# Performance work log

Hardware: AMD Instinct MI355X
Metric: run time of the kernel (lower is better)

## Reference

```python
import jax, jax.numpy as jnp
import numpy as np


def setup_inputs() -> dict:
    key = jax.random.key(0)
    ks = jax.random.split(key, 8)
    B, C, H, W = 4, 256, 64, 64
    C8 = C // 8
    s = 0.05
    return {
        "x": jax.random.normal(ks[0], (B, C, H, W), jnp.float32),
        "wq": jax.random.normal(ks[1], (C8, C), jnp.float32) * s,
        "bq": jax.random.normal(ks[2], (C8,), jnp.float32) * s,
        "wk": jax.random.normal(ks[3], (C8, C), jnp.float32) * s,
        "bk": jax.random.normal(ks[4], (C8,), jnp.float32) * s,
        "wv": jax.random.normal(ks[5], (C, C), jnp.float32) * s,
        "bv": jax.random.normal(ks[6], (C,), jnp.float32) * s,
        "gamma": jax.random.uniform(ks[7], (1,), jnp.float32),
    }


def reference(x, wq, bq, wk, bk, wv, bv, gamma):
    B, C, H, W = x.shape
    N = H * W
    xf = x.reshape(B, C, N)  # flatten spatial: [B, C, N]
    # 1x1 convs are channel-wise matmuls
    q = jnp.einsum("dc,bcn->bnd", wq, xf) + bq[None, None, :]  # [B, N, C/8]
    k = jnp.einsum("dc,bcn->bdn", wk, xf) + bk[None, :, None]  # [B, C/8, N]
    v = jnp.einsum("dc,bcn->bdn", wv, xf) + bv[None, :, None]  # [B, C, N]
    energy = jnp.einsum("bnd,bdm->bnm", q, k)  # [B, N, N]
    attention = jax.nn.softmax(energy, axis=-1)
    # out = value @ attention^T  -> [B, C, N]
    out = jnp.einsum("bcm,bnm->bcn", v, attention)
    out = out.reshape(B, C, H, W)
    return gamma[0] * out + x
```

## Files before the change

### kernel.cpp

```cpp
#include <hip/hip_runtime.h>
#include <hip/hip_bf16.h>
#include <stdint.h>

#define B_ 4
#define C_ 256
#define N_ 4096
#define D_ 32
#define KT 256

typedef __bf16 bf16_t;
typedef __bf16 bf16x4_t __attribute__((ext_vector_type(4)));
typedef __bf16 bf16x8_t __attribute__((ext_vector_type(8)));
typedef float  f32x4    __attribute__((ext_vector_type(4)));

__global__ __launch_bounds__(256) void cast_kernel(
    const float* __restrict__ x,
    const float* __restrict__ wq, const float* __restrict__ wk,
    const float* __restrict__ wv,
    bf16_t* __restrict__ xbT, bf16_t* __restrict__ Wb)
{
  const int bid = blockIdx.x;
  const int t = threadIdx.x;
  if (bid >= 1024) {
    const int gr = bid - 1024;
    float v;
    if (gr < 32)      v = wq[gr * C_ + t];
    else if (gr < 64) v = wk[(gr - 32) * C_ + t];
    else              v = wv[(gr - 64) * C_ + t];
    Wb[gr * C_ + t] = (bf16_t)v;
    return;
  }
  __shared__ float xs[64][65];
  const int n0 = (bid & 63) * 64;
  const int c0 = ((bid >> 6) & 3) * 64;
  const int b  = bid >> 8;

  const int lr = t >> 4;
  const int lc = (t & 15) * 4;
#pragma unroll
  for (int i = 0; i < 4; ++i) {
    const f32x4 v = *(const f32x4*)(x + ((size_t)(b * C_ + c0 + lr + i * 16)) * N_ + n0 + lc);
    xs[lr + i * 16][lc + 0] = v[0];
    xs[lr + i * 16][lc + 1] = v[1];
    xs[lr + i * 16][lc + 2] = v[2];
    xs[lr + i * 16][lc + 3] = v[3];
  }
  __syncthreads();
  const int nr = t >> 2;
  const int cb = (t & 3) * 16;
  bf16_t tmp[16];
#pragma unroll
  for (int j = 0; j < 16; ++j) tmp[j] = (bf16_t)xs[cb + j][nr];
  bf16_t* dst = xbT + ((size_t)(b * N_ + n0 + nr)) * C_ + c0 + cb;
  *(bf16x8_t*)dst       = *(bf16x8_t*)&tmp[0];
  *(bf16x8_t*)(dst + 8) = *(bf16x8_t*)&tmp[8];
}

__global__ __launch_bounds__(256) void proj_kernel(
    const bf16_t* __restrict__ Wb, const bf16_t* __restrict__ xbT,
    const float* __restrict__ bq, const float* __restrict__ bk,
    const float* __restrict__ bv,
    bf16_t* __restrict__ Qh, bf16_t* __restrict__ Kh, bf16_t* __restrict__ Vh)
{
  const int bi = blockIdx.x;
  const int b  = bi & 3;
  const int n0 = (bi >> 2) * 64;
  const int t = threadIdx.x, w = t >> 6, lane = t & 63;
  const int l4 = lane >> 4, lm = lane & 15;

  const f32x4 z4 = {0.f, 0.f, 0.f, 0.f};
  f32x4 acc[5][4];
#pragma unroll
  for (int rt = 0; rt < 5; ++rt)
#pragma unroll
    for (int ct = 0; ct < 4; ++ct) acc[rt][ct] = z4;

#pragma unroll 1
  for (int k0 = 0; k0 < C_; k0 += 64) {
    bf16x8_t af[5][2], bfr[4][2];
#pragma unroll
    for (int rt = 0; rt < 5; ++rt)
#pragma unroll
      for (int kc = 0; kc < 2; ++kc)
        af[rt][kc] = *(const bf16x8_t*)(Wb + (size_t)(w * 80 + rt * 16 + lm) * C_ + k0 + kc * 32 + l4 * 8);
#pragma unroll
    for (int ct = 0; ct < 4; ++ct)
#pragma unroll
      for (int kc = 0; kc < 2; ++kc)
        bfr[ct][kc] = *(const bf16x8_t*)(xbT + ((size_t)(b * N_ + n0 + ct * 16 + lm)) * C_ + k0 + kc * 32 + l4 * 8);
#pragma unroll
    for (int rt = 0; rt < 5; ++rt)
#pragma unroll
      for (int ct = 0; ct < 4; ++ct)
#pragma unroll
        for (int kc = 0; kc < 2; ++kc)
          acc[rt][ct] = __builtin_amdgcn_mfma_f32_16x16x32_bf16(af[rt][kc], bfr[ct][kc], acc[rt][ct], 0, 0, 0);
  }

#pragma unroll
  for (int rt = 0; rt < 5; ++rt)
#pragma unroll
    for (int r = 0; r < 4; ++r) {
      const int gr = w * 80 + rt * 16 + 4 * l4 + r;
      const float bias = (gr < 32) ? bq[gr] : (gr < 64) ? bk[gr - 32] : bv[gr - 64];
#pragma unroll
      for (int ct = 0; ct < 4; ++ct) {
        const int n = n0 + ct * 16 + lm;
        float v = acc[rt][ct][r] + bias;
        if (gr < 32) {
          v *= 1.44269504088896f;
          Qh[((size_t)(b * N_ + n)) * D_ + gr] = (bf16_t)v;
        } else if (gr < 64) {
          Kh[((size_t)(b * N_ + n)) * D_ + (gr - 32)] = (bf16_t)v;
        } else {
          Vh[((size_t)(b * C_ + (gr - 64))) * N_ + n] = (bf16_t)v;
        }
      }
    }
}

__global__ __launch_bounds__(512, 2) void attn_kernel(
    const bf16_t* __restrict__ Qh, const bf16_t* __restrict__ Kh,
    const bf16_t* __restrict__ Vh, const float* __restrict__ x,
    const float* __restrict__ gamma, float* __restrict__ out)
{
  __shared__ __align__(16) bf16_t Pl[2][64][KT];
  __shared__ __align__(16) float  Lx[64][12];

  const int bi = blockIdx.x;
  const int xcd = bi & 7, slot = bi >> 3;
  const int b  = xcd >> 1;
  const int q0 = ((xcd & 1) * 32 + slot) * 64;

  const int t = threadIdx.x, w = t >> 6, lane = t & 63;
  const int l4 = lane >> 4, lm = lane & 15;
  const int swz = (lm & 7) << 3;

  const f32x4 z4 = {0.f, 0.f, 0.f, 0.f};

  bf16x8_t qf[4];
#pragma unroll
  for (int rt = 0; rt < 4; ++rt)
    qf[rt] = *(const bf16x8_t*)(Qh + ((size_t)(b * N_ + q0 + rt * 16 + lm)) * D_ + l4 * 8);

  const bf16_t* kbase = Kh + ((size_t)(b * N_ + w * 32 + lm)) * D_ + l4 * 8;
  const bf16_t* vbase = Vh + ((size_t)(b * C_ + w * 32 + lm)) * N_ + l4 * 8;

  f32x4 acc[2][4];
#pragma unroll
  for (int ct = 0; ct < 2; ++ct)
#pragma unroll
    for (int rt = 0; rt < 4; ++rt) acc[ct][rt] = z4;
  float l_run[4] = {0.f, 0.f, 0.f, 0.f};

  bf16x8_t kf[2], kn[2];
#pragma unroll
  for (int mt = 0; mt < 2; ++mt)
    kf[mt] = *(const bf16x8_t*)(kbase + (size_t)(mt * 16) * D_);
  bf16x8_t vf0[2][2], vf1[2][2];
#pragma unroll
  for (int ct = 0; ct < 2; ++ct)
#pragma unroll
    for (int kc = 0; kc < 2; ++kc) {
      vf0[ct][kc] = *(const bf16x8_t*)(vbase + (size_t)(ct * 16) * N_ + kc * 32);
      vf1[ct][kc] = *(const bf16x8_t*)(vbase + (size_t)(ct * 16) * N_ + 64 + kc * 32);
    }

#pragma unroll 1
  for (int it = 0; it < N_ / KT; ++it) {
    const int buf = it & 1;

    f32x4 S[4][2];
#pragma unroll
    for (int rt = 0; rt < 4; ++rt)
#pragma unroll
      for (int mt = 0; mt < 2; ++mt)
        S[rt][mt] = __builtin_amdgcn_mfma_f32_16x16x32_bf16(kf[mt], qf[rt], z4, 0, 0, 0);

    const int k0n = ((it + 1) * KT) & (N_ - 1);
#pragma unroll
    for (int mt = 0; mt < 2; ++mt)
      kn[mt] = *(const bf16x8_t*)(kbase + (size_t)(k0n + mt * 16) * D_);

#pragma unroll
    for (int rt = 0; rt < 4; ++rt) {
      const int prow = rt * 16 + lm;
#pragma unroll
      for (int mt = 0; mt < 2; ++mt) {
        const float p0 = __builtin_amdgcn_exp2f(S[rt][mt][0]);
        const float p1 = __builtin_amdgcn_exp2f(S[rt][mt][1]);
        const float p2 = __builtin_amdgcn_exp2f(S[rt][mt][2]);
        const float p3 = __builtin_amdgcn_exp2f(S[rt][mt][3]);
        l_run[rt] += (p0 + p1) + (p2 + p3);
        bf16x4_t w4 = {(bf16_t)p0, (bf16_t)p1, (bf16_t)p2, (bf16_t)p3};
        *(bf16x4_t*)&Pl[buf][prow][(w * 32 + mt * 16 + 4 * l4) ^ swz] = w4;
      }
    }

    asm volatile("s_waitcnt lgkmcnt(0)" ::: "memory");
    __builtin_amdgcn_s_barrier();

#pragma unroll
    for (int s4 = 0; s4 < 4; ++s4) {
      bf16x8_t pa[4][2];
#pragma unroll
      for (int rt = 0; rt < 4; ++rt)
#pragma unroll
        for (int kc = 0; kc < 2; ++kc)
          pa[rt][kc] = *(const bf16x8_t*)&Pl[buf][rt * 16 + lm][(s4 * 64 + kc * 32 + l4 * 8) ^ swz];
      const int knx = (it * KT + (s4 + 2) * 64) & (N_ - 1);
      if ((s4 & 1) == 0) {
#pragma unroll
        for (int ct = 0; ct < 2; ++ct)
#pragma unroll
          for (int kc = 0; kc < 2; ++kc)
#pragma unroll
            for (int rt = 0; rt < 4; ++rt)
              acc[ct][rt] = __builtin_amdgcn_mfma_f32_16x16x32_bf16(vf0[ct][kc], pa[rt][kc], acc[ct][rt], 0, 0, 0);
#pragma unroll
        for (int ct = 0; ct < 2; ++ct)
#pragma unroll
          for (int kc = 0; kc < 2; ++kc)
            vf0[ct][kc] = *(const bf16x8_t*)(vbase + (size_t)(ct * 16) * N_ + knx + kc * 32);
      } else {
#pragma unroll
        for (int ct = 0; ct < 2; ++ct)
#pragma unroll
          for (int kc = 0; kc < 2; ++kc)
#pragma unroll
            for (int rt = 0; rt < 4; ++rt)
              acc[ct][rt] = __builtin_amdgcn_mfma_f32_16x16x32_bf16(vf1[ct][kc], pa[rt][kc], acc[ct][rt], 0, 0, 0);
#pragma unroll
        for (int ct = 0; ct < 2; ++ct)
#pragma unroll
          for (int kc = 0; kc < 2; ++kc)
            vf1[ct][kc] = *(const bf16x8_t*)(vbase + (size_t)(ct * 16) * N_ + knx + kc * 32);
      }
    }

#pragma unroll
    for (int mt = 0; mt < 2; ++mt) kf[mt] = kn[mt];
  }

#pragma unroll
  for (int rt = 0; rt < 4; ++rt) {
    l_run[rt] += __shfl_xor(l_run[rt], 16);
    l_run[rt] += __shfl_xor(l_run[rt], 32);
  }
  if (l4 == 0) {
#pragma unroll
    for (int rt = 0; rt < 4; ++rt) Lx[rt * 16 + lm][w] = l_run[rt];
  }
  asm volatile("s_waitcnt lgkmcnt(0)" ::: "memory");
  __builtin_amdgcn_s_barrier();

  const float g = gamma[0];
#pragma unroll
  for (int rt = 0; rt < 4; ++rt) {
    const f32x4 s0 = *(const f32x4*)&Lx[rt * 16 + lm][0];
    const f32x4 s1 = *(const f32x4*)&Lx[rt * 16 + lm][4];
    const float lt = ((s0[0] + s0[1]) + (s0[2] + s0[3])) + ((s1[0] + s1[1]) + (s1[2] + s1[3]));
    const float inv = 1.f / lt;
    const int n = q0 + rt * 16 + lm;
#pragma unroll
    for (int ct = 0; ct < 2; ++ct) {
#pragma unroll
      for (int r = 0; r < 4; ++r) {
        const int c = w * 32 + ct * 16 + 4 * l4 + r;
        const size_t idx = ((size_t)(b * C_ + c)) * N_ + n;
        out[idx] = g * (acc[ct][rt][r] * inv) + x[idx];
      }
    }
  }
}

extern "C" void kernel_launch(void* const* d_in, const int* in_sizes, int n_in,
                              void* d_out, int out_size, void* d_ws, size_t ws_size,
                              hipStream_t stream) {
  const float* x     = (const float*)d_in[0];
  const float* wq    = (const float*)d_in[1];
  const float* bq    = (const float*)d_in[2];
  const float* wk    = (const float*)d_in[3];
  const float* bk    = (const float*)d_in[4];
  const float* wv    = (const float*)d_in[5];
  const float* bv    = (const float*)d_in[6];
  const float* gamma = (const float*)d_in[7];
  float* out = (float*)d_out;

  bf16_t* Qh  = (bf16_t*)d_ws;
  bf16_t* Kh  = Qh + (size_t)B_ * N_ * D_;
  bf16_t* Vh  = Kh + (size_t)B_ * N_ * D_;
  bf16_t* Wb  = Vh + (size_t)B_ * C_ * N_;
  bf16_t* xbT = Wb + (size_t)320 * C_;

  cast_kernel<<<1344, 256, 0, stream>>>(x, wq, wk, wv, xbT, Wb);
  proj_kernel<<<256, 256, 0, stream>>>(Wb, xbT, bq, bk, bv, Qh, Kh, Vh);
  attn_kernel<<<256, 512, 0, stream>>>(Qh, Kh, Vh, x, gamma, out);
}
```

Baseline: 94.84 us.

## Split attention key range in two and combine partial outputs

Splits the key dimension into two halves so attention launches 512 blocks instead of 256, each covering half the keys. Every block writes a bf16 normalized partial output and its row sums, and a new combine kernel merges the two halves weighted by those sums, then applies gamma and the residual. The aim is more blocks per device and higher occupancy (launch bounds raised to 4 per CU). The cost is an extra kernel launch, extra global traffic for the partials, and bf16 rounding of the intermediate output.

```diff
diff --git a/kernel.cpp b/kernel.cpp
--- a/kernel.cpp
+++ b/kernel.cpp
@@ -7,6 +7,7 @@
 #define N_ 4096
 #define D_ 32
 #define KT 256
+#define KH 2048
 
 typedef __bf16 bf16_t;
 typedef __bf16 bf16x4_t __attribute__((ext_vector_type(4)));
@@ -119,18 +120,20 @@
     }
 }
 
-__global__ __launch_bounds__(512, 2) void attn_kernel(
+__global__ __launch_bounds__(512, 4) void attn_kernel(
     const bf16_t* __restrict__ Qh, const bf16_t* __restrict__ Kh,
-    const bf16_t* __restrict__ Vh, const float* __restrict__ x,
-    const float* __restrict__ gamma, float* __restrict__ out)
+    const bf16_t* __restrict__ Vh,
+    bf16_t* __restrict__ opart, float* __restrict__ lpart)
 {
   __shared__ __align__(16) bf16_t Pl[2][64][KT];
   __shared__ __align__(16) float  Lx[64][12];
 
   const int bi = blockIdx.x;
-  const int xcd = bi & 7, slot = bi >> 3;
+  const int xcd = bi & 7;
   const int b  = xcd >> 1;
-  const int q0 = ((xcd & 1) * 32 + slot) * 64;
+  const int kh = xcd & 1;
+  const int qt = bi >> 3;
+  const int q0 = qt * 64;
 
   const int t = threadIdx.x, w = t >> 6, lane = t & 63;
   const int l4 = lane >> 4, lm = lane & 15;
@@ -143,8 +146,8 @@
   for (int rt = 0; rt < 4; ++rt)
     qf[rt] = *(const bf16x8_t*)(Qh + ((size_t)(b * N_ + q0 + rt * 16 + lm)) * D_ + l4 * 8);
 
-  const bf16_t* kbase = Kh + ((size_t)(b * N_ + w * 32 + lm)) * D_ + l4 * 8;
-  const bf16_t* vbase = Vh + ((size_t)(b * C_ + w * 32 + lm)) * N_ + l4 * 8;
+  const bf16_t* kbase = Kh + ((size_t)(b * N_ + kh * KH + w * 32 + lm)) * D_ + l4 * 8;
+  const bf16_t* vbase = Vh + ((size_t)(b * C_ + w * 32 + lm)) * N_ + kh * KH + l4 * 8;
 
   f32x4 acc[2][4];
 #pragma unroll
@@ -167,7 +170,7 @@
     }
 
 #pragma unroll 1
-  for (int it = 0; it < N_ / KT; ++it) {
+  for (int it = 0; it < KH / KT; ++it) {
     const int buf = it & 1;
 
     f32x4 S[4][2];
@@ -177,7 +180,7 @@
       for (int mt = 0; mt < 2; ++mt)
         S[rt][mt] = __builtin_amdgcn_mfma_f32_16x16x32_bf16(kf[mt], qf[rt], z4, 0, 0, 0);
 
-    const int k0n = ((it + 1) * KT) & (N_ - 1);
+    const int k0n = ((it + 1) * KT) & (KH - 1);
 #pragma unroll
     for (int mt = 0; mt < 2; ++mt)
       kn[mt] = *(const bf16x8_t*)(kbase + (size_t)(k0n + mt * 16) * D_);
@@ -208,7 +211,7 @@
 #pragma unroll
         for (int kc = 0; kc < 2; ++kc)
           pa[rt][kc] = *(const bf16x8_t*)&Pl[buf][rt * 16 + lm][(s4 * 64 + kc * 32 + l4 * 8) ^ swz];
-      const int knx = (it * KT + (s4 + 2) * 64) & (N_ - 1);
+      const int knx = (it * KT + (s4 + 2) * 64) & (KH - 1);
       if ((s4 & 1) == 0) {
 #pragma unroll
         for (int ct = 0; ct < 2; ++ct)
@@ -254,24 +257,65 @@
   asm volatile("s_waitcnt lgkmcnt(0)" ::: "memory");
   __builtin_amdgcn_s_barrier();
 
-  const float g = gamma[0];
+  const int blk = xcd * 64 + qt;
+  bf16_t* oblk = opart + (size_t)blk * (C_ * 64);
 #pragma unroll
   for (int rt = 0; rt < 4; ++rt) {
     const f32x4 s0 = *(const f32x4*)&Lx[rt * 16 + lm][0];
     const f32x4 s1 = *(const f32x4*)&Lx[rt * 16 + lm][4];
     const float lt = ((s0[0] + s0[1]) + (s0[2] + s0[3])) + ((s1[0] + s1[1]) + (s1[2] + s1[3]));
     const float inv = 1.f / lt;
-    const int n = q0 + rt * 16 + lm;
+    const int nl = rt * 16 + lm;
+    if (w == 0 && l4 == 0) lpart[blk * 64 + nl] = lt;
 #pragma unroll
     for (int ct = 0; ct < 2; ++ct) {
 #pragma unroll
       for (int r = 0; r < 4; ++r) {
         const int c = w * 32 + ct * 16 + 4 * l4 + r;
-        const size_t idx = ((size_t)(b * C_ + c)) * N_ + n;
-        out[idx] = g * (acc[ct][rt][r] * inv) + x[idx];
+        oblk[c * 64 + nl] = (bf16_t)(acc[ct][rt][r] * inv);
       }
     }
   }
+}
+
+__global__ __launch_bounds__(256) void combine_kernel(
+    const bf16_t* __restrict__ opart, const float* __restrict__ lpart,
+    const float* __restrict__ x, const float* __restrict__ gamma,
+    float* __restrict__ out)
+{
+  const int g  = blockIdx.x * 256 + threadIdx.x;
+  const int e  = g * 8;
+  const int b  = e >> 20;
+  const int c  = (e >> 12) & 255;
+  const int n  = e & 4095;
+  const int qt = n >> 6;
+  const int nl = n & 63;
+  const int blkA = (b * 2) * 64 + qt;
+  const int blkB = blkA + 64;
+
+  const bf16x8_t oA = *(const bf16x8_t*)(opart + (size_t)blkA * (C_ * 64) + c * 64 + nl);
+  const bf16x8_t oB = *(const bf16x8_t*)(opart + (size_t)blkB * (C_ * 64) + c * 64 + nl);
+  const f32x4 lA0 = *(const f32x4*)(lpart + blkA * 64 + nl);
+  const f32x4 lA1 = *(const f32x4*)(lpart + blkA * 64 + nl + 4);
+  const f32x4 lB0 = *(const f32x4*)(lpart + blkB * 64 + nl);
+  const f32x4 lB1 = *(const f32x4*)(lpart + blkB * 64 + nl + 4);
+  const float gm = gamma[0];
+
+  const f32x4 xv0 = *(const f32x4*)(x + e);
+  const f32x4 xv1 = *(const f32x4*)(x + e + 4);
+  f32x4 o0, o1;
+#pragma unroll
+  for (int j = 0; j < 4; ++j) {
+    const float la = lA0[j], lb = lB0[j];
+    o0[j] = gm * ((la * (float)oA[j] + lb * (float)oB[j]) / (la + lb)) + xv0[j];
+  }
+#pragma unroll
+  for (int j = 0; j < 4; ++j) {
+    const float la = lA1[j], lb = lB1[j];
+    o1[j] = gm * ((la * (float)oA[4 + j] + lb * (float)oB[4 + j]) / (la + lb)) + xv1[j];
+  }
+  *(f32x4*)(out + e)     = o0;
+  *(f32x4*)(out + e + 4) = o1;
 }
 
 extern "C" void kernel_launch(void* const* d_in, const int* in_sizes, int n_in,
@@ -287,13 +331,16 @@
   const float* gamma = (const float*)d_in[7];
   float* out = (float*)d_out;
 
-  bf16_t* Qh  = (bf16_t*)d_ws;
-  bf16_t* Kh  = Qh + (size_t)B_ * N_ * D_;
-  bf16_t* Vh  = Kh + (size_t)B_ * N_ * D_;
-  bf16_t* Wb  = Vh + (size_t)B_ * C_ * N_;
-  bf16_t* xbT = Wb + (size_t)320 * C_;
+  bf16_t* Qh    = (bf16_t*)d_ws;
+  bf16_t* Kh    = Qh + (size_t)B_ * N_ * D_;
+  bf16_t* Vh    = Kh + (size_t)B_ * N_ * D_;
+  bf16_t* Wb    = Vh + (size_t)B_ * C_ * N_;
+  bf16_t* xbT   = Wb + (size_t)320 * C_;
+  bf16_t* opart = xbT + (size_t)B_ * N_ * C_;
+  float*  lpart = (float*)(opart + (size_t)512 * C_ * 64);
 
   cast_kernel<<<1344, 256, 0, stream>>>(x, wq, wk, wv, xbT, Wb);
   proj_kernel<<<256, 256, 0, stream>>>(Wb, xbT, bq, bk, bv, Qh, Kh, Vh);
-  attn_kernel<<<256, 512, 0, stream>>>(Qh, Kh, Vh, x, gamma, out);
-}
+  attn_kernel<<<512, 512, 0, stream>>>(Qh, Kh, Vh, opart, lpart);
+  combine_kernel<<<2048, 256, 0, stream>>>(opart, lpart, x, gamma, out);
+}
```

Result: slower. 132.9 us (+40.1%).

## Fuse x transpose-cast into projection kernel and double attention key tile

Applied to the files above, without the earlier changes.

Removes the standalone transpose/cast of x to a bf16 N-major buffer. The projection kernel now stages each 64x64 fp32 tile of x in shared memory and builds its bf16 MFMA operands from there, which drops one full global write and read of the transposed input. Separately, the attention key tile grows from 256 to 512 keys per iteration, with each wave handling 64 keys. That halves the number of barrier-separated iterations, at the cost of a larger shared P buffer and more score registers per wave. The extra register and LDS pressure could hurt occupancy or cause spills.

```diff
diff --git a/kernel.cpp b/kernel.cpp
--- a/kernel.cpp
+++ b/kernel.cpp
@@ -6,62 +6,33 @@
 #define C_ 256
 #define N_ 4096
 #define D_ 32
-#define KT 256
+#define KT 512
 
 typedef __bf16 bf16_t;
 typedef __bf16 bf16x4_t __attribute__((ext_vector_type(4)));
 typedef __bf16 bf16x8_t __attribute__((ext_vector_type(8)));
 typedef float  f32x4    __attribute__((ext_vector_type(4)));
 
-__global__ __launch_bounds__(256) void cast_kernel(
-    const float* __restrict__ x,
+__global__ __launch_bounds__(256) void cast_w_kernel(
     const float* __restrict__ wq, const float* __restrict__ wk,
-    const float* __restrict__ wv,
-    bf16_t* __restrict__ xbT, bf16_t* __restrict__ Wb)
+    const float* __restrict__ wv, bf16_t* __restrict__ Wb)
 {
-  const int bid = blockIdx.x;
-  const int t = threadIdx.x;
-  if (bid >= 1024) {
-    const int gr = bid - 1024;
-    float v;
-    if (gr < 32)      v = wq[gr * C_ + t];
-    else if (gr < 64) v = wk[(gr - 32) * C_ + t];
-    else              v = wv[(gr - 64) * C_ + t];
-    Wb[gr * C_ + t] = (bf16_t)v;
-    return;
-  }
-  __shared__ float xs[64][65];
-  const int n0 = (bid & 63) * 64;
-  const int c0 = ((bid >> 6) & 3) * 64;
-  const int b  = bid >> 8;
-
-  const int lr = t >> 4;
-  const int lc = (t & 15) * 4;
-#pragma unroll
-  for (int i = 0; i < 4; ++i) {
-    const f32x4 v = *(const f32x4*)(x + ((size_t)(b * C_ + c0 + lr + i * 16)) * N_ + n0 + lc);
-    xs[lr + i * 16][lc + 0] = v[0];
-    xs[lr + i * 16][lc + 1] = v[1];
-    xs[lr + i * 16][lc + 2] = v[2];
-    xs[lr + i * 16][lc + 3] = v[3];
-  }
-  __syncthreads();
-  const int nr = t >> 2;
-  const int cb = (t & 3) * 16;
-  bf16_t tmp[16];
-#pragma unroll
-  for (int j = 0; j < 16; ++j) tmp[j] = (bf16_t)xs[cb + j][nr];
-  bf16_t* dst = xbT + ((size_t)(b * N_ + n0 + nr)) * C_ + c0 + cb;
-  *(bf16x8_t*)dst       = *(bf16x8_t*)&tmp[0];
-  *(bf16x8_t*)(dst + 8) = *(bf16x8_t*)&tmp[8];
+  const int gr = blockIdx.x;
+  const int t  = threadIdx.x;
+  float v;
+  if (gr < 32)      v = wq[gr * C_ + t];
+  else if (gr < 64) v = wk[(gr - 32) * C_ + t];
+  else              v = wv[(gr - 64) * C_ + t];
+  Wb[gr * C_ + t] = (bf16_t)v;
 }
 
 __global__ __launch_bounds__(256) void proj_kernel(
-    const bf16_t* __restrict__ Wb, const bf16_t* __restrict__ xbT,
+    const float* __restrict__ x, const bf16_t* __restrict__ Wb,
     const float* __restrict__ bq, const float* __restrict__ bk,
     const float* __restrict__ bv,
     bf16_t* __restrict__ Qh, bf16_t* __restrict__ Kh, bf16_t* __restrict__ Vh)
 {
+  __shared__ float xs[64][65];
   const int bi = blockIdx.x;
   const int b  = bi & 3;
   const int n0 = (bi >> 2) * 64;
@@ -75,8 +46,22 @@
 #pragma unroll
     for (int ct = 0; ct < 4; ++ct) acc[rt][ct] = z4;
 
+  const int lr = t >> 2;
+  const int lc = (t & 3) * 16;
+
 #pragma unroll 1
   for (int k0 = 0; k0 < C_; k0 += 64) {
+    __syncthreads();
+#pragma unroll
+    for (int i = 0; i < 4; ++i) {
+      const f32x4 v = *(const f32x4*)(x + ((size_t)(b * C_ + k0 + lr)) * N_ + n0 + lc + i * 4);
+      xs[lr][lc + i * 4 + 0] = v[0];
+      xs[lr][lc + i * 4 + 1] = v[1];
+      xs[lr][lc + i * 4 + 2] = v[2];
+      xs[lr][lc + i * 4 + 3] = v[3];
+    }
+    __syncthreads();
+
     bf16x8_t af[5][2], bfr[4][2];
 #pragma unroll
     for (int rt = 0; rt < 5; ++rt)
@@ -86,8 +71,13 @@
 #pragma unroll
     for (int ct = 0; ct < 4; ++ct)
 #pragma unroll
-      for (int kc = 0; kc < 2; ++kc)
-        bfr[ct][kc] = *(const bf16x8_t*)(xbT + ((size_t)(b * N_ + n0 + ct * 16 + lm)) * C_ + k0 + kc * 32 + l4 * 8);
+      for (int kc = 0; kc < 2; ++kc) {
+        bf16_t tmp[8];
+#pragma unroll
+        for (int j = 0; j < 8; ++j)
+          tmp[j] = (bf16_t)xs[kc * 32 + l4 * 8 + j][ct * 16 + lm];
+        bfr[ct][kc] = *(bf16x8_t*)tmp;
+      }
 #pragma unroll
     for (int rt = 0; rt < 5; ++rt)
 #pragma unroll
@@ -143,7 +133,7 @@
   for (int rt = 0; rt < 4; ++rt)
     qf[rt] = *(const bf16x8_t*)(Qh + ((size_t)(b * N_ + q0 + rt * 16 + lm)) * D_ + l4 * 8);
 
-  const bf16_t* kbase = Kh + ((size_t)(b * N_ + w * 32 + lm)) * D_ + l4 * 8;
+  const bf16_t* kbase = Kh + ((size_t)(b * N_ + w * 64 + lm)) * D_ + l4 * 8;
   const bf16_t* vbase = Vh + ((size_t)(b * C_ + w * 32 + lm)) * N_ + l4 * 8;
 
   f32x4 acc[2][4];
@@ -153,9 +143,9 @@
     for (int rt = 0; rt < 4; ++rt) acc[ct][rt] = z4;
   float l_run[4] = {0.f, 0.f, 0.f, 0.f};
 
-  bf16x8_t kf[2], kn[2];
-#pragma unroll
-  for (int mt = 0; mt < 2; ++mt)
+  bf16x8_t kf[4], kn[4];
+#pragma unroll
+  for (int mt = 0; mt < 4; ++mt)
     kf[mt] = *(const bf16x8_t*)(kbase + (size_t)(mt * 16) * D_);
   bf16x8_t vf0[2][2], vf1[2][2];
 #pragma unroll
@@ -170,30 +160,30 @@
   for (int it = 0; it < N_ / KT; ++it) {
     const int buf = it & 1;
 
-    f32x4 S[4][2];
+    f32x4 S[4][4];
 #pragma unroll
     for (int rt = 0; rt < 4; ++rt)
 #pragma unroll
-      for (int mt = 0; mt < 2; ++mt)
+      for (int mt = 0; mt < 4; ++mt)
         S[rt][mt] = __builtin_amdgcn_mfma_f32_16x16x32_bf16(kf[mt], qf[rt], z4, 0, 0, 0);
 
     const int k0n = ((it + 1) * KT) & (N_ - 1);
 #pragma unroll
-    for (int mt = 0; mt < 2; ++mt)
+    for (int mt = 0; mt < 4; ++mt)
       kn[mt] = *(const bf16x8_t*)(kbase + (size_t)(k0n + mt * 16) * D_);
 
 #pragma unroll
     for (int rt = 0; rt < 4; ++rt) {
       const int prow = rt * 16 + lm;
 #pragma unroll
-      for (int mt = 0; mt < 2; ++mt) {
+      for (int mt = 0; mt < 4; ++mt) {
         const float p0 = __builtin_amdgcn_exp2f(S[rt][mt][0]);
         const float p1 = __builtin_amdgcn_exp2f(S[rt][mt][1]);
         const float p2 = __builtin_amdgcn_exp2f(S[rt][mt][2]);
         const float p3 = __builtin_amdgcn_exp2f(S[rt][mt][3]);
         l_run[rt] += (p0 + p1) + (p2 + p3);
         bf16x4_t w4 = {(bf16_t)p0, (bf16_t)p1, (bf16_t)p2, (bf16_t)p3};
-        *(bf16x4_t*)&Pl[buf][prow][(w * 32 + mt * 16 + 4 * l4) ^ swz] = w4;
+        *(bf16x4_t*)&Pl[buf][prow][(w * 64 + mt * 16 + 4 * l4) ^ swz] = w4;
       }
     }
 
@@ -201,7 +191,7 @@
     __builtin_amdgcn_s_barrier();
 
 #pragma unroll
-    for (int s4 = 0; s4 < 4; ++s4) {
+    for (int s4 = 0; s4 < 8; ++s4) {
       bf16x8_t pa[4][2];
 #pragma unroll
       for (int rt = 0; rt < 4; ++rt)
@@ -239,7 +229,7 @@
     }
 
 #pragma unroll
-    for (int mt = 0; mt < 2; ++mt) kf[mt] = kn[mt];
+    for (int mt = 0; mt < 4; ++mt) kf[mt] = kn[mt];
   }
 
 #pragma unroll
@@ -287,13 +277,12 @@
   const float* gamma = (const float*)d_in[7];
   float* out = (float*)d_out;
 
-  bf16_t* Qh  = (bf16_t*)d_ws;
-  bf16_t* Kh  = Qh + (size_t)B_ * N_ * D_;
-  bf16_t* Vh  = Kh + (size_t)B_ * N_ * D_;
-  bf16_t* Wb  = Vh + (size_t)B_ * C_ * N_;
-  bf16_t* xbT = Wb + (size_t)320 * C_;
-
-  cast_kernel<<<1344, 256, 0, stream>>>(x, wq, wk, wv, xbT, Wb);
-  proj_kernel<<<256, 256, 0, stream>>>(Wb, xbT, bq, bk, bv, Qh, Kh, Vh);
+  bf16_t* Qh = (bf16_t*)d_ws;
+  bf16_t* Kh = Qh + (size_t)B_ * N_ * D_;
+  bf16_t* Vh = Kh + (size_t)B_ * N_ * D_;
+  bf16_t* Wb = Vh + (size_t)B_ * C_ * N_;
+
+  cast_w_kernel<<<320, 256, 0, stream>>>(wq, wk, wv, Wb);
+  proj_kernel<<<256, 256, 0, stream>>>(x, Wb, bq, bk, bv, Qh, Kh, Vh);
   attn_kernel<<<256, 512, 0, stream>>>(Qh, Kh, Vh, x, gamma, out);
 }
```

Measured after the change: 93.12 us, median of 2. No clear change (-1.8%).
